# Optimization experiments

Hardware: AMD Instinct MI355X
Metric: run time of the kernel (lower is better)

The kernel has to match this reference:

```python
import jax, jax.numpy as jnp
import numpy as np


def _nac_weight(w_hat, m_hat):
    # NeuralAccumulatorCell effective weight: tanh(W_hat) * sigmoid(M_hat)
    return jnp.tanh(w_hat) * jax.nn.sigmoid(m_hat)


def setup_inputs() -> dict:
    key = jax.random.key(0)
    ks = jax.random.split(key, 7)
    S = 511        # len(init_state)
    D_IN = 1 + S   # 512
    N_STEPS = 262144
    N_TERMS = 32
    return {
        "X": jax.random.normal(ks[0], (S,), dtype=jnp.float32),
        "W_hat1": jax.random.normal(ks[1], (128, D_IN), dtype=jnp.float32),
        "M_hat1": jax.random.normal(ks[2], (128, D_IN), dtype=jnp.float32),
        "W_hat2": jax.random.normal(ks[3], (32, 128), dtype=jnp.float32),
        "M_hat2": jax.random.normal(ks[4], (32, 128), dtype=jnp.float32),
        "W_hat3": jax.random.normal(ks[5], (N_TERMS, 32), dtype=jnp.float32),
        "M_hat3": jax.random.normal(ks[6], (N_TERMS, 32), dtype=jnp.float32),
        "n_steps": N_STEPS,
    }


def reference(X, W_hat1, M_hat1, W_hat2, M_hat2, W_hat3, M_hat3, n_steps):
    # Original loop builds per-step input [t/n_steps, *state] with state fixed
    # across the loop, so all steps batch into one input matrix.
    n = jnp.float32(n_steps)
    t = jnp.arange(n_steps, dtype=jnp.float32) / n            # [T]
    state = jnp.broadcast_to(X[None, :], (n_steps, X.shape[0]))  # [T, S]
    x_in = jnp.concatenate([t[:, None], state], axis=1)       # [T, 1+S]
    W1 = _nac_weight(W_hat1, M_hat1)
    W2 = _nac_weight(W_hat2, M_hat2)
    W3 = _nac_weight(W_hat3, M_hat3)
    h = x_in @ W1.T     # [T, 128]
    h = h @ W2.T        # [T, 32]
    y = h @ W3.T        # [T, n_terms]
    return y
```

## Files before the change

### kernel.cpp

```cpp
#include <hip/hip_runtime.h>
#include <math.h>


__device__ __forceinline__ float nac_w_fast(float wh, float mh) {
    float t = 1.0f - 2.0f / (__expf(2.0f * wh) + 1.0f);
    float s = 1.0f / (1.0f + __expf(-mh));
    return t * s;
}

__global__ __launch_bounds__(1024) void fp_coef(
        const float* __restrict__ X,
        const float* __restrict__ W1, const float* __restrict__ M1,
        const float* __restrict__ W2, const float* __restrict__ M2,
        const float* __restrict__ W3, const float* __restrict__ M3,
        float* __restrict__ ws) {
    __shared__ float sX[512];
    __shared__ float sA[128], sB[128];
    __shared__ float s2A[32], s2B[32];
    const int tid = threadIdx.x;
    const int wave = tid >> 6;
    const int lane = tid & 63;

    if (tid < 512) sX[tid] = (tid == 0) ? 0.0f : X[tid - 1];
    __syncthreads();

    #pragma unroll
    for (int r = 0; r < 8; ++r) {
        const int k = wave * 8 + r;
        const float* w1r = W1 + k * 512;
        const float* m1r = M1 + k * 512;
        float p = 0.0f;
        float w0 = 0.0f;
        #pragma unroll
        for (int m = 0; m < 8; ++m) {
            const int c = lane + m * 64;
            float w = nac_w_fast(w1r[c], m1r[c]);
            if (m == 0 && lane == 0) w0 = w;
            p = fmaf(w, sX[c], p);
        }
        #pragma unroll
        for (int d = 32; d >= 1; d >>= 1) p += __shfl_xor(p, d, 64);
        if (lane == 0) { sA[k] = w0; sB[k] = p; }
    }
    __syncthreads();

    #pragma unroll
    for (int r = 0; r < 2; ++r) {
        const int k = wave * 2 + r;
        float wA = nac_w_fast(W2[k * 128 + lane],      M2[k * 128 + lane]);
        float wB = nac_w_fast(W2[k * 128 + 64 + lane], M2[k * 128 + 64 + lane]);
        float pa = wA * sA[lane] + wB * sA[64 + lane];
        float pb = wA * sB[lane] + wB * sB[64 + lane];
        #pragma unroll
        for (int d = 32; d >= 1; d >>= 1) {
            pa += __shfl_xor(pa, d, 64);
            pb += __shfl_xor(pb, d, 64);
        }
        if (lane == 0) { s2A[k] = pa; s2B[k] = pb; }
    }
    __syncthreads();

    #pragma unroll
    for (int r = 0; r < 2; ++r) {
        const int k = wave * 2 + r;
        const int col = lane & 31;
        float w = nac_w_fast(W3[k * 32 + col], M3[k * 32 + col]);
        float pa = w * s2A[col];
        float pb = w * s2B[col];
        #pragma unroll
        for (int d = 16; d >= 1; d >>= 1) {
            pa += __shfl_xor(pa, d, 32);
            pb += __shfl_xor(pb, d, 32);
        }
        if (lane == 0) { ws[k] = pa; ws[32 + k] = pb; }
    }
}

__global__ __launch_bounds__(256) void fp_writer(
        const float* __restrict__ coef,
        float* __restrict__ out,
        int T, float inv_n) {
    __shared__ float sA[32], sB[32];
    const int tid = threadIdx.x;
    if (tid < 32) { sA[tid] = coef[tid]; sB[tid] = coef[32 + tid]; }
    __syncthreads();

    const int total = T * 8;
    const int stride = gridDim.x * blockDim.x;
    int idx = blockIdx.x * blockDim.x + tid;
    if (idx >= total) return;
    const int g = idx & 7;
    const int j = g * 4;
    const float a0 = sA[j], a1 = sA[j + 1], a2 = sA[j + 2], a3 = sA[j + 3];
    const float b0 = sB[j], b1 = sB[j + 1], b2 = sB[j + 2], b3 = sB[j + 3];
    float4* __restrict__ out4 = reinterpret_cast<float4*>(out);
    for (; idx < total; idx += stride) {
        const float tv = (float)(idx >> 3) * inv_n;
        float4 o;
        o.x = fmaf(tv, a0, b0);
        o.y = fmaf(tv, a1, b1);
        o.z = fmaf(tv, a2, b2);
        o.w = fmaf(tv, a3, b3);
        out4[idx] = o;
    }
}

extern "C" void kernel_launch(void* const* d_in, const int* in_sizes, int n_in,
                              void* d_out, int out_size, void* d_ws, size_t ws_size,
                              hipStream_t stream) {
    const float* X  = (const float*)d_in[0];
    const float* W1 = (const float*)d_in[1];
    const float* M1 = (const float*)d_in[2];
    const float* W2 = (const float*)d_in[3];
    const float* M2 = (const float*)d_in[4];
    const float* W3 = (const float*)d_in[5];
    const float* M3 = (const float*)d_in[6];
    float* out = (float*)d_out;
    float* ws  = (float*)d_ws;

    const int T = out_size / 32;
    const float inv_n = 1.0f / (float)T;

    fp_coef<<<1, 1024, 0, stream>>>(X, W1, M1, W2, M2, W3, M3, ws);

    const int total = T * 8;
    int blocks = (total + 255) / 256;
    if (blocks > 2048) blocks = 2048;
    fp_writer<<<blocks, 256, 0, stream>>>(ws, out, T, inv_n);
}
```

Before: 102.4 us.

## Split first-layer coefficient reduction across 128 blocks with separate small-layer kernel

Stage one of the coefficient computation (a 128x512 NAC weight and dot product with X) now runs as its own kernel with one 512-thread block per output row, instead of inside a single 1024-thread block. A second single-block, 256-thread kernel then computes layers two and three from workspace results, with loop trip counts adjusted for four waves. The aim is to spread the 512 KB weight read and the transcendental work over many compute units rather than one. The cost is an extra kernel launch and a round-trip of intermediates through global memory.

Result: faster. 93.58 us (-8.6%).

```diff
diff --git a/kernel.cpp b/kernel.cpp
--- a/kernel.cpp
+++ b/kernel.cpp
@@ -8,45 +8,48 @@
     return t * s;
 }
 
-__global__ __launch_bounds__(1024) void fp_coef(
+__global__ __launch_bounds__(512) void fp_s1(
         const float* __restrict__ X,
         const float* __restrict__ W1, const float* __restrict__ M1,
+        float* __restrict__ ws) {
+    const int k = blockIdx.x;
+    const int j = threadIdx.x;
+    const int idx = k * 512 + j;
+    float w = nac_w_fast(W1[idx], M1[idx]);
+    float xv = (j == 0) ? 0.0f : X[j - 1];
+    float p = w * xv;
+    #pragma unroll
+    for (int d = 32; d >= 1; d >>= 1) p += __shfl_xor(p, d, 64);
+    __shared__ float red[8];
+    const int wave = j >> 6;
+    if ((j & 63) == 0) red[wave] = p;
+    __syncthreads();
+    if (j == 0) {
+        float bsum = 0.0f;
+        #pragma unroll
+        for (int w8 = 0; w8 < 8; ++w8) bsum += red[w8];
+        ws[k] = w;
+        ws[128 + k] = bsum;
+    }
+}
+
+__global__ __launch_bounds__(256) void fp_s23(
         const float* __restrict__ W2, const float* __restrict__ M2,
         const float* __restrict__ W3, const float* __restrict__ M3,
         float* __restrict__ ws) {
-    __shared__ float sX[512];
     __shared__ float sA[128], sB[128];
     __shared__ float s2A[32], s2B[32];
     const int tid = threadIdx.x;
     const int wave = tid >> 6;
     const int lane = tid & 63;
 
-    if (tid < 512) sX[tid] = (tid == 0) ? 0.0f : X[tid - 1];
+    if (tid < 128) sA[tid] = ws[tid];
+    else           sB[tid - 128] = ws[tid];
     __syncthreads();
 
     #pragma unroll
     for (int r = 0; r < 8; ++r) {
         const int k = wave * 8 + r;
-        const float* w1r = W1 + k * 512;
-        const float* m1r = M1 + k * 512;
-        float p = 0.0f;
-        float w0 = 0.0f;
-        #pragma unroll
-        for (int m = 0; m < 8; ++m) {
-            const int c = lane + m * 64;
-            float w = nac_w_fast(w1r[c], m1r[c]);
-            if (m == 0 && lane == 0) w0 = w;
-            p = fmaf(w, sX[c], p);
-        }
-        #pragma unroll
-        for (int d = 32; d >= 1; d >>= 1) p += __shfl_xor(p, d, 64);
-        if (lane == 0) { sA[k] = w0; sB[k] = p; }
-    }
-    __syncthreads();
-
-    #pragma unroll
-    for (int r = 0; r < 2; ++r) {
-        const int k = wave * 2 + r;
         float wA = nac_w_fast(W2[k * 128 + lane],      M2[k * 128 + lane]);
         float wB = nac_w_fast(W2[k * 128 + 64 + lane], M2[k * 128 + 64 + lane]);
         float pa = wA * sA[lane] + wB * sA[64 + lane];
@@ -61,8 +64,8 @@
     __syncthreads();
 
     #pragma unroll
-    for (int r = 0; r < 2; ++r) {
-        const int k = wave * 2 + r;
+    for (int r = 0; r < 8; ++r) {
+        const int k = wave * 8 + r;
         const int col = lane & 31;
         float w = nac_w_fast(W3[k * 32 + col], M3[k * 32 + col]);
         float pa = w * s2A[col];
@@ -72,7 +75,7 @@
             pa += __shfl_xor(pa, d, 32);
             pb += __shfl_xor(pb, d, 32);
         }
-        if (lane == 0) { ws[k] = pa; ws[32 + k] = pb; }
+        if (lane == 0) { ws[256 + k] = pa; ws[288 + k] = pb; }
     }
 }
 
@@ -121,10 +124,11 @@
     const int T = out_size / 32;
     const float inv_n = 1.0f / (float)T;
 
-    fp_coef<<<1, 1024, 0, stream>>>(X, W1, M1, W2, M2, W3, M3, ws);
+    fp_s1<<<128, 512, 0, stream>>>(X, W1, M1, ws);
+    fp_s23<<<1, 256, 0, stream>>>(W2, M2, W3, M3, ws);
 
     const int total = T * 8;
     int blocks = (total + 255) / 256;
     if (blocks > 2048) blocks = 2048;
-    fp_writer<<<blocks, 256, 0, stream>>>(ws, out, T, inv_n);
+    fp_writer<<<blocks, 256, 0, stream>>>(ws + 256, out, T, inv_n);
 }
```
